# Optimization experiments

Measured on AMD Instinct MI355X. Metric: run time of the kernel, lower is better.

## Reference

```python
import jax, jax.numpy as jnp
import numpy as np

EPS = 1e-5  # BatchNorm1d default eps
DIMS = [(784, 1024), (1024, 1024), (1024, 1024), (1024, 10)]


def setup_inputs() -> dict:
    key = jax.random.key(0)
    ks = jax.random.split(key, 25)
    d = {"x": jax.random.normal(ks[0], (32768, 784), jnp.float32)}
    for i, (fi, fo) in enumerate(DIMS):
        j = i + 1
        base = 1 + 6 * i
        d[f"W{j}"] = jax.random.uniform(ks[base], (fo, fi), jnp.float32, -1.0, 1.0)
        d[f"b{j}"] = jnp.full((fo,), 0.01, jnp.float32)
        d[f"gamma{j}"] = jax.random.uniform(ks[base + 1], (fo,), jnp.float32, 0.5, 1.5)
        d[f"beta{j}"] = 0.1 * jax.random.normal(ks[base + 2], (fo,), jnp.float32)
        d[f"mean{j}"] = 0.1 * jax.random.normal(ks[base + 3], (fo,), jnp.float32)
        d[f"var{j}"] = jax.random.uniform(ks[base + 4], (fo,), jnp.float32, 0.5, 1.5)
    return d


def _bn(h, gamma, beta, mean, var):
    # inference-mode BatchNorm1d with running stats
    return gamma * (h - mean) * jax.lax.rsqrt(var + EPS) + beta


def reference(x,
              W1, b1, gamma1, beta1, mean1, var1,
              W2, b2, gamma2, beta2, mean2, var2,
              W3, b3, gamma3, beta3, mean3, var3,
              W4, b4, gamma4, beta4, mean4, var4):
    h = x.reshape(-1, 784)
    # layer 1: Quantizer(1) -> BinarizeLinear -> BN -> Hardtanh
    h = jnp.sign(h)
    h = h @ jnp.sign(W1).T + b1
    h = jnp.clip(_bn(h, gamma1, beta1, mean1, var1), -1.0, 1.0)
    # layer 2
    h = jnp.sign(h)
    h = h @ jnp.sign(W2).T + b2
    h = jnp.clip(_bn(h, gamma2, beta2, mean2, var2), -1.0, 1.0)
    # layer 3
    h = jnp.sign(h)
    h = h @ jnp.sign(W3).T + b3
    h = jnp.clip(_bn(h, gamma3, beta3, mean3, var3), -1.0, 1.0)
    # layer 4: Quantizer -> BinarizeLinear -> BN (no hardtanh)
    h = jnp.sign(h)
    h = h @ jnp.sign(W4).T + b4
    return _bn(h, gamma4, beta4, mean4, var4)
```

## Files before the change

### kernel.cpp

```cpp
#include <hip/hip_runtime.h>
#include <cstdint>
#include <climits>


typedef __attribute__((ext_vector_type(4))) int i32x4_t;

__device__ __forceinline__ void gload_lds16(const void* g, void* l) {
  __builtin_amdgcn_global_load_lds(
      (const __attribute__((address_space(1))) unsigned int*)g,
      (__attribute__((address_space(3))) unsigned int*)l, 16, 0, 0);
}

__device__ __forceinline__ int pack4(const float4 v) {
  int b0 = v.x > 0.f ? 1 : (v.x < 0.f ? -1 : 0);
  int b1 = v.y > 0.f ? 1 : (v.y < 0.f ? -1 : 0);
  int b2 = v.z > 0.f ? 1 : (v.z < 0.f ? -1 : 0);
  int b3 = v.w > 0.f ? 1 : (v.w < 0.f ? -1 : 0);
  return (b0 & 0xff) | ((b1 & 0xff) << 8) | ((b2 & 0xff) << 16) | (b3 << 24);
}


__global__ __launch_bounds__(256) void prep_mega_kernel(
    const float* __restrict__ x, int8_t* __restrict__ A0,
    const float* __restrict__ W1f, const float* __restrict__ W2f,
    const float* __restrict__ W3f, const float* __restrict__ W4f,
    int8_t* __restrict__ Wp1, int8_t* __restrict__ Wp2,
    int8_t* __restrict__ Wp3, int8_t* __restrict__ Wp4,
    const float* b1, const float* g1, const float* be1, const float* m1, const float* v1,
    const float* b2, const float* g2, const float* be2, const float* m2, const float* v2,
    const float* b3, const float* g3, const float* be3, const float* m3, const float* v3,
    const float* b4, const float* g4, const float* be4, const float* m4, const float* v4,
    int* __restrict__ T1, int* __restrict__ T2, int* __restrict__ T3,
    int8_t* __restrict__ S1, int8_t* __restrict__ S2, int8_t* __restrict__ S3,
    float* __restrict__ sc4, float* __restrict__ of4) {
  const int b = blockIdx.x;
  const int t = threadIdx.x;
  if (b < 32768) {
    const int col = t * 4;
    if (col < 784) {
      int packed = pack4(*(const float4*)(x + (size_t)b * 784 + col));
      *(int*)(A0 + (size_t)b * 832 + col) = packed;
    } else if (col < 832) {
      *(int*)(A0 + (size_t)b * 832 + col) = 0;
    }
  } else if (b < 35968) {
    const int b2i = b - 32768;
    const float* Wf; int8_t* Wp; int N, K, n, ost;
    if (b2i < 1024)      { Wf = W1f; Wp = Wp1; N = 1024; K = 784;  n = b2i;        ost = 832;  }
    else if (b2i < 2048) { Wf = W2f; Wp = Wp2; N = 1024; K = 1024; n = b2i - 1024; ost = 1024; }
    else if (b2i < 3072) { Wf = W3f; Wp = Wp3; N = 1024; K = 1024; n = b2i - 2048; ost = 1024; }
    else                 { Wf = W4f; Wp = Wp4; N = 10;   K = 1024; n = b2i - 3072; ost = 1024; }
    const int col = t * 4;
    if (col < ost) {
      int packed = 0;
      if (n < N && col + 3 < K)
        packed = pack4(*(const float4*)(Wf + (size_t)n * K + col));
      *(int*)(Wp + (size_t)n * ost + col) = packed;
    }
  } else {
    const int pb = b - 35968;
    if (pb < 12) {
      const int layer = pb >> 2;
      const int n = (pb & 3) * 256 + t;
      const float *bb, *gg, *be, *me, *va; int* T; int8_t* S;
      if (layer == 0)      { bb = b1; gg = g1; be = be1; me = m1; va = v1; T = T1; S = S1; }
      else if (layer == 1) { bb = b2; gg = g2; be = be2; me = m2; va = v2; T = T2; S = S2; }
      else                 { bb = b3; gg = g3; be = be3; me = m3; va = v3; T = T3; S = S3; }
      double g = (double)gg[n];
      double rs = 1.0 / sqrt((double)va[n] + 1e-5);
      int th; int8_t s;
      if (g > 0.0) {
        double tv = (double)me[n] - (double)bb[n] - (double)be[n] / (g * rs);
        tv = fmin(fmax(tv, -2.0e9), 2.0e9);
        th = (int)floor(tv) + 1; s = 1;
      } else if (g < 0.0) {
        double tv = (double)me[n] - (double)bb[n] - (double)be[n] / (g * rs);
        tv = fmin(fmax(tv, -2.0e9), 2.0e9);
        th = (int)ceil(tv); s = -1;
      } else {
        th = INT_MIN; s = (be[n] > 0.f) ? (int8_t)1 : (int8_t)-1;
      }
      T[n] = th; S[n] = s;
    } else if (t < 10) {
      double rs = 1.0 / sqrt((double)v4[t] + 1e-5);
      double sd = (double)g4[t] * rs;
      sc4[t] = (float)sd;
      of4[t] = (float)(sd * ((double)b4[t] - (double)m4[t]) + (double)be4[t]);
    }
  }
}

template <int FINAL>
__global__ __launch_bounds__(256) void gemm_bnn_kernel(
    const int8_t* __restrict__ A, const int8_t* __restrict__ W,
    int ldk, int nkt,
    const int* __restrict__ T, const int8_t* __restrict__ S,
    const float* __restrict__ scale, const float* __restrict__ offs,
    int8_t* __restrict__ Aout, float* __restrict__ out) {
  __shared__ i32x4_t smem[2048];
  int8_t* sm = (int8_t*)smem;
  const int tid = threadIdx.x;
  const int lane = tid & 63;
  const int w = tid >> 6;
  const int wrow = w >> 1, wcol = w & 1;
  const int row0 = blockIdx.x * 128;
  const int col0 = blockIdx.y * 128;

  const int jj0 = tid, jj1 = tid + 256;
  const int r0 = jj0 >> 2, r1 = jj1 >> 2;
  const int s0 = (jj0 & 3) ^ ((r0 >> 1) & 3);
  const int s1 = (jj1 & 3) ^ ((r1 >> 1) & 3);
  const int8_t* aS0 = A + (size_t)(row0 + r0) * ldk + s0 * 16;
  const int8_t* aS1 = A + (size_t)(row0 + r1) * ldk + s1 * 16;
  const int8_t* bS0 = W + (size_t)(col0 + r0) * ldk + s0 * 16;
  const int8_t* bS1 = W + (size_t)(col0 + r1) * ldk + s1 * 16;
  const int dA0 = jj0 * 16, dA1 = jj1 * 16;
  const int dB0 = 8192 + jj0 * 16, dB1 = 8192 + jj1 * 16;

  int a_off[4], b_off[4];
#pragma unroll
  for (int i = 0; i < 4; ++i) {
    int ra = wrow * 64 + i * 16 + (lane & 15);
    a_off[i] = ra * 64 + ((((lane >> 4) ^ (ra >> 1)) & 3) << 4);
    int rb = wcol * 64 + i * 16 + (lane & 15);
    b_off[i] = 8192 + rb * 64 + ((((lane >> 4) ^ (rb >> 1)) & 3) << 4);
  }

  i32x4_t acc[4][4];
#pragma unroll
  for (int m = 0; m < 4; ++m)
#pragma unroll
    for (int n = 0; n < 4; ++n) acc[m][n] = (i32x4_t){0, 0, 0, 0};

  gload_lds16(aS0, sm + dA0);
  gload_lds16(aS1, sm + dA1);
  gload_lds16(bS0, sm + dB0);
  gload_lds16(bS1, sm + dB1);

  for (int kt = 0; kt < nkt - 1; ++kt) {
    aS0 += 64; aS1 += 64; bS0 += 64; bS1 += 64;
    int8_t* smw = sm + (((kt + 1) & 1) << 14);
    gload_lds16(aS0, smw + dA0);
    gload_lds16(aS1, smw + dA1);
    gload_lds16(bS0, smw + dB0);
    gload_lds16(bS1, smw + dB1);
    asm volatile("s_waitcnt vmcnt(4)" ::: "memory");
    __builtin_amdgcn_s_barrier();
    const int8_t* smr = sm + ((kt & 1) << 14);
    i32x4_t av[4], bv[4];
#pragma unroll
    for (int i = 0; i < 4; ++i) av[i] = *(const i32x4_t*)(smr + a_off[i]);
#pragma unroll
    for (int i = 0; i < 4; ++i) bv[i] = *(const i32x4_t*)(smr + b_off[i]);
#pragma unroll
    for (int m = 0; m < 4; ++m)
#pragma unroll
      for (int n = 0; n < 4; ++n)
        acc[m][n] = __builtin_amdgcn_mfma_i32_16x16x64_i8(av[m], bv[n], acc[m][n], 0, 0, 0);
    __builtin_amdgcn_s_barrier();
  }
  asm volatile("s_waitcnt vmcnt(0)" ::: "memory");
  __builtin_amdgcn_s_barrier();
  {
    const int8_t* smr = sm + (((nkt - 1) & 1) << 14);
    i32x4_t av[4], bv[4];
#pragma unroll
    for (int i = 0; i < 4; ++i) av[i] = *(const i32x4_t*)(smr + a_off[i]);
#pragma unroll
    for (int i = 0; i < 4; ++i) bv[i] = *(const i32x4_t*)(smr + b_off[i]);
#pragma unroll
    for (int m = 0; m < 4; ++m)
#pragma unroll
      for (int n = 0; n < 4; ++n)
        acc[m][n] = __builtin_amdgcn_mfma_i32_16x16x64_i8(av[m], bv[n], acc[m][n], 0, 0, 0);
  }

  if (FINAL == 0) {
#pragma unroll
    for (int n = 0; n < 4; ++n) {
      const int oc = col0 + wcol * 64 + n * 16 + (lane & 15);
      const int tn = T[oc];
      const int8_t sn = S[oc];
#pragma unroll
      for (int m = 0; m < 4; ++m) {
        const int orb = row0 + wrow * 64 + m * 16 + ((lane >> 4) << 2);
#pragma unroll
        for (int r = 0; r < 4; ++r) {
          int8_t v = (acc[m][n][r] >= tn) ? sn : (int8_t)(-sn);
          Aout[(size_t)(orb + r) * 1024 + oc] = v;
        }
      }
    }
  } else {
#pragma unroll
    for (int n = 0; n < 4; ++n) {
      const int oc = col0 + wcol * 64 + n * 16 + (lane & 15);
      if (oc < 10) {
        const float sc = scale[oc], of = offs[oc];
#pragma unroll
        for (int m = 0; m < 4; ++m) {
          const int orb = row0 + wrow * 64 + m * 16 + ((lane >> 4) << 2);
#pragma unroll
          for (int r = 0; r < 4; ++r)
            out[(size_t)(orb + r) * 10 + oc] = sc * (float)acc[m][n][r] + of;
        }
      }
    }
  }
}


#define A0_STRIDE 28

__global__ __launch_bounds__(256) void pack_w_kernel(
    const float* __restrict__ W, uint32_t* __restrict__ Wp,
    int nout, int K, int wstride) {
  int idx = blockIdx.x * blockDim.x + threadIdx.x;
  if (idx >= nout * wstride) return;
  int n = idx / wstride;
  int wi = idx - n * wstride;
  const float* wr = W + (size_t)n * K;
  uint32_t word = 0;
  int base = wi * 32;
  for (int i = 0; i < 32; ++i) {
    int c = base + i;
    if (c < K && wr[c] > 0.f) word |= (1u << i);
  }
  Wp[idx] = word;
}

__global__ __launch_bounds__(256) void prep_thr_kernel(
    const float* __restrict__ b, const float* __restrict__ gamma,
    const float* __restrict__ beta, const float* __restrict__ mean,
    const float* __restrict__ var, int K, int N,
    int* __restrict__ thr, uint32_t* __restrict__ flipm) {
  int n = blockIdx.x * blockDim.x + threadIdx.x;
  if (n >= N) return;
  double g = (double)gamma[n];
  double rs = 1.0 / sqrt((double)var[n] + 1e-5);
  int th;
  if (g != 0.0) {
    double t = (double)mean[n] - (double)b[n] - (double)beta[n] / (g * rs);
    double pt = ((double)K - t) * 0.5;
    th = (g > 0.0) ? (int)ceil(pt) : ((int)floor(pt) + 1);
  } else {
    th = (beta[n] > 0.f) ? (K + 2) : -1;
  }
  thr[n] = th;
  if ((n & 31) == 0) {
    uint32_t m = 0;
    for (int i = 0; i < 32 && (n + i) < N; ++i)
      if (gamma[n + i] < 0.f) m |= (1u << i);
    flipm[n >> 5] = m;
  }
}

__global__ __launch_bounds__(64) void prep_out_kernel(
    const float* __restrict__ b, const float* __restrict__ gamma,
    const float* __restrict__ beta, const float* __restrict__ mean,
    const float* __restrict__ var, int N,
    float* __restrict__ s, float* __restrict__ o) {
  int n = threadIdx.x;
  if (n >= N) return;
  double rs = 1.0 / sqrt((double)var[n] + 1e-5);
  double sd = (double)gamma[n] * rs;
  s[n] = (float)sd;
  o[n] = (float)(sd * ((double)b[n] - (double)mean[n]) + (double)beta[n]);
}

__global__ __launch_bounds__(256) void pack_a_kernel(
    const float* __restrict__ x, uint32_t* __restrict__ A0) {
  int gt = blockIdx.x * blockDim.x + threadIdx.x;
  int wv = gt >> 6;
  int lane = gt & 63;
  int row = wv / 13;
  int seg = wv - row * 13;
  int col = (seg << 6) + lane;
  bool pred = (col < 784) && (x[(size_t)row * 784 + col] > 0.f);
  unsigned long long m = __ballot(pred);
  int widx = seg * 2;
  if (lane == 0)
    A0[(size_t)row * A0_STRIDE + widx] = (uint32_t)m;
  else if (lane == 1 && widx + 1 < 25)
    A0[(size_t)row * A0_STRIDE + widx + 1] = (uint32_t)(m >> 32);
}

__device__ __forceinline__ void layer1024(
    uint32_t a[32], const uint32_t* __restrict__ Wp,
    const int* __restrict__ thr, const uint32_t* __restrict__ fm,
    uint32_t* lds, int lane, int w) {
  const int nb = w * 128;
  uint32_t word = 0;
#pragma unroll 2
  for (int ni = 0; ni < 128; ++ni) {
    const int n = nb + ni;
    const uint32_t* __restrict__ wp = Wp + n * 32;
    uint32_t p0 = 0, p1 = 0, p2 = 0, p3 = 0;
#pragma unroll
    for (int k = 0; k < 32; k += 4) {
      p0 += __popc(a[k + 0] ^ wp[k + 0]);
      p1 += __popc(a[k + 1] ^ wp[k + 1]);
      p2 += __popc(a[k + 2] ^ wp[k + 2]);
      p3 += __popc(a[k + 3] ^ wp[k + 3]);
    }
    int p = (int)(p0 + p1 + p2 + p3);
    word |= ((p < thr[n]) ? 1u : 0u) << (ni & 31);
    if ((ni & 31) == 31) {
      lds[lane * 33 + (n >> 5)] = word ^ fm[n >> 5];
      word = 0;
    }
  }
  __syncthreads();
#pragma unroll
  for (int k = 0; k < 32; ++k) a[k] = lds[lane * 33 + k];
  __syncthreads();
}

__global__ __launch_bounds__(512, 4) void fused_kernel(
    const uint32_t* __restrict__ A0,
    const uint32_t* __restrict__ Wp1, const int* __restrict__ thr1, const uint32_t* __restrict__ fm1,
    const uint32_t* __restrict__ Wp2, const int* __restrict__ thr2, const uint32_t* __restrict__ fm2,
    const uint32_t* __restrict__ Wp3, const int* __restrict__ thr3, const uint32_t* __restrict__ fm3,
    const uint32_t* __restrict__ Wp4, const float* __restrict__ s4, const float* __restrict__ o4,
    float* __restrict__ out) {
  __shared__ uint32_t lds[64 * 33];
  const int lane = threadIdx.x & 63;
  const int w = __builtin_amdgcn_readfirstlane((int)(threadIdx.x >> 6));
  const int row = blockIdx.x * 64 + lane;

  uint32_t a[32];
  {
    const uint4* A4 = (const uint4*)(A0 + (size_t)row * A0_STRIDE);
#pragma unroll
    for (int i = 0; i < 7; ++i) {
      uint4 q = A4[i];
      a[4 * i + 0] = q.x; a[4 * i + 1] = q.y; a[4 * i + 2] = q.z; a[4 * i + 3] = q.w;
    }
  }
  {
    const int nb = w * 128;
    uint32_t word = 0;
#pragma unroll 2
    for (int ni = 0; ni < 128; ++ni) {
      const int n = nb + ni;
      const uint32_t* __restrict__ wp = Wp1 + n * A0_STRIDE;
      uint32_t p0 = 0, p1 = 0, p2 = 0, p3 = 0;
#pragma unroll
      for (int k = 0; k < 24; k += 4) {
        p0 += __popc(a[k + 0] ^ wp[k + 0]);
        p1 += __popc(a[k + 1] ^ wp[k + 1]);
        p2 += __popc(a[k + 2] ^ wp[k + 2]);
        p3 += __popc(a[k + 3] ^ wp[k + 3]);
      }
      p0 += __popc(a[24] ^ wp[24]);
      int p = (int)(p0 + p1 + p2 + p3);
      word |= ((p < thr1[n]) ? 1u : 0u) << (ni & 31);
      if ((ni & 31) == 31) {
        lds[lane * 33 + (n >> 5)] = word ^ fm1[n >> 5];
        word = 0;
      }
    }
    __syncthreads();
#pragma unroll
    for (int k = 0; k < 32; ++k) a[k] = lds[lane * 33 + k];
    __syncthreads();
  }
  layer1024(a, Wp2, thr2, fm2, lds, lane, w);
  layer1024(a, Wp3, thr3, fm3, lds, lane, w);
  for (int j = w; j < 10; j += 8) {
    const uint32_t* __restrict__ wp = Wp4 + j * 32;
    uint32_t p0 = 0, p1 = 0, p2 = 0, p3 = 0;
#pragma unroll
    for (int k = 0; k < 32; k += 4) {
      p0 += __popc(a[k + 0] ^ wp[k + 0]);
      p1 += __popc(a[k + 1] ^ wp[k + 1]);
      p2 += __popc(a[k + 2] ^ wp[k + 2]);
      p3 += __popc(a[k + 3] ^ wp[k + 3]);
    }
    float dotf = 1024.f - 2.f * (float)(p0 + p1 + p2 + p3);
    out[(size_t)row * 10 + j] = s4[j] * dotf + o4[j];
  }
}

extern "C" void kernel_launch(void* const* d_in, const int* in_sizes, int n_in,
                              void* d_out, int out_size, void* d_ws, size_t ws_size,
                              hipStream_t stream) {
  const float* x   = (const float*)d_in[0];
  const float* W1  = (const float*)d_in[1];
  const float* b1  = (const float*)d_in[2];
  const float* g1  = (const float*)d_in[3];
  const float* be1 = (const float*)d_in[4];
  const float* m1  = (const float*)d_in[5];
  const float* v1  = (const float*)d_in[6];
  const float* W2  = (const float*)d_in[7];
  const float* b2  = (const float*)d_in[8];
  const float* g2  = (const float*)d_in[9];
  const float* be2 = (const float*)d_in[10];
  const float* m2  = (const float*)d_in[11];
  const float* v2  = (const float*)d_in[12];
  const float* W3  = (const float*)d_in[13];
  const float* b3  = (const float*)d_in[14];
  const float* g3  = (const float*)d_in[15];
  const float* be3 = (const float*)d_in[16];
  const float* m3  = (const float*)d_in[17];
  const float* v3  = (const float*)d_in[18];
  const float* W4  = (const float*)d_in[19];
  const float* b4  = (const float*)d_in[20];
  const float* g4  = (const float*)d_in[21];
  const float* be4 = (const float*)d_in[22];
  const float* m4  = (const float*)d_in[23];
  const float* v4  = (const float*)d_in[24];
  float* outp = (float*)d_out;
  (void)in_sizes; (void)n_in; (void)out_size;

  uint8_t* ws = (uint8_t*)d_ws;
  const size_t NEED = 100ULL << 20;

  if (ws_size >= NEED) {
    size_t off = 0;
    int8_t* A0  = (int8_t*)(ws + off); off += (size_t)32768 * 832;
    int8_t* Bp1 = (int8_t*)(ws + off); off += (size_t)32768 * 1024;
    int8_t* Bp2 = (int8_t*)(ws + off); off += (size_t)32768 * 1024;
    int8_t* Wp1 = (int8_t*)(ws + off); off += (size_t)1024 * 832;
    int8_t* Wp2 = (int8_t*)(ws + off); off += (size_t)1024 * 1024;
    int8_t* Wp3 = (int8_t*)(ws + off); off += (size_t)1024 * 1024;
    int8_t* Wp4 = (int8_t*)(ws + off); off += (size_t)128 * 1024;
    int* T1     = (int*)(ws + off);    off += 4096;
    int* T2     = (int*)(ws + off);    off += 4096;
    int* T3     = (int*)(ws + off);    off += 4096;
    int8_t* S1  = (int8_t*)(ws + off); off += 1024;
    int8_t* S2  = (int8_t*)(ws + off); off += 1024;
    int8_t* S3  = (int8_t*)(ws + off); off += 1024;
    float* sc4  = (float*)(ws + off);  off += 512;
    float* of4  = (float*)(ws + off);  off += 512;

    prep_mega_kernel<<<35981, 256, 0, stream>>>(
        x, A0, W1, W2, W3, W4, Wp1, Wp2, Wp3, Wp4,
        b1, g1, be1, m1, v1, b2, g2, be2, m2, v2,
        b3, g3, be3, m3, v3, b4, g4, be4, m4, v4,
        T1, T2, T3, S1, S2, S3, sc4, of4);

    gemm_bnn_kernel<0><<<dim3(256, 8), 256, 0, stream>>>(
        A0, Wp1, 832, 13, T1, S1, nullptr, nullptr, Bp1, nullptr);
    gemm_bnn_kernel<0><<<dim3(256, 8), 256, 0, stream>>>(
        Bp1, Wp2, 1024, 16, T2, S2, nullptr, nullptr, Bp2, nullptr);
    gemm_bnn_kernel<0><<<dim3(256, 8), 256, 0, stream>>>(
        Bp2, Wp3, 1024, 16, T3, S3, nullptr, nullptr, Bp1, nullptr);
    gemm_bnn_kernel<1><<<dim3(256, 1), 256, 0, stream>>>(
        Bp1, Wp4, 1024, 16, nullptr, nullptr, sc4, of4, nullptr, outp);
  } else {
    size_t off = 0;
    uint32_t* A0  = (uint32_t*)(ws + off); off += (size_t)32768 * A0_STRIDE * 4;
    uint32_t* Wp1 = (uint32_t*)(ws + off); off += (size_t)1024 * A0_STRIDE * 4;
    uint32_t* Wp2 = (uint32_t*)(ws + off); off += (size_t)1024 * 32 * 4;
    uint32_t* Wp3 = (uint32_t*)(ws + off); off += (size_t)1024 * 32 * 4;
    uint32_t* Wp4 = (uint32_t*)(ws + off); off += 4096;
    int* thr1     = (int*)(ws + off);      off += 4096;
    int* thr2     = (int*)(ws + off);      off += 4096;
    int* thr3     = (int*)(ws + off);      off += 4096;
    uint32_t* fm1 = (uint32_t*)(ws + off); off += 128;
    uint32_t* fm2 = (uint32_t*)(ws + off); off += 128;
    uint32_t* fm3 = (uint32_t*)(ws + off); off += 128;
    float* s4o    = (float*)(ws + off);    off += 64;
    float* o4o    = (float*)(ws + off);    off += 64;

    pack_w_kernel<<<(1024 * A0_STRIDE + 255) / 256, 256, 0, stream>>>(W1, Wp1, 1024, 784, A0_STRIDE);
    pack_w_kernel<<<(1024 * 32 + 255) / 256, 256, 0, stream>>>(W2, Wp2, 1024, 1024, 32);
    pack_w_kernel<<<(1024 * 32 + 255) / 256, 256, 0, stream>>>(W3, Wp3, 1024, 1024, 32);
    pack_w_kernel<<<(10 * 32 + 255) / 256, 256, 0, stream>>>(W4, Wp4, 10, 1024, 32);
    prep_thr_kernel<<<4, 256, 0, stream>>>(b1, g1, be1, m1, v1, 784, 1024, thr1, fm1);
    prep_thr_kernel<<<4, 256, 0, stream>>>(b2, g2, be2, m2, v2, 1024, 1024, thr2, fm2);
    prep_thr_kernel<<<4, 256, 0, stream>>>(b3, g3, be3, m3, v3, 1024, 1024, thr3, fm3);
    prep_out_kernel<<<1, 64, 0, stream>>>(b4, g4, be4, m4, v4, 10, s4o, o4o);
    pack_a_kernel<<<(32768 * 13) / 4, 256, 0, stream>>>(x, A0);
    fused_kernel<<<512, 512, 0, stream>>>(A0, Wp1, thr1, fm1, Wp2, thr2, fm2,
                                          Wp3, thr3, fm3, Wp4, s4o, o4o, outp);
  }
}
```

Before: 345.8 us.

## Use 256x256 tiles with 512-thread blocks and grid swizzle for hidden BNN GEMMs

Replaces the 128x128-tile int8 MFMA GEMM for the three hidden layers with a 256x256-tile kernel of 8 waves, each computing a 128x64 sub-tile, using double-buffered 64 KB LDS. A block-index swizzle groups blocks that share A rows and W columns to improve L2 reuse. The larger tiles halve global/LDS traffic per MFMA but raise register pressure (32 accumulators per wave) and cut the grid to 512 blocks, which may lower occupancy. The final layer is split into its own non-templated kernel.

```diff
diff --git a/kernel.cpp b/kernel.cpp
--- a/kernel.cpp
+++ b/kernel.cpp
@@ -90,13 +90,117 @@
   }
 }
 
-template <int FINAL>
-__global__ __launch_bounds__(256) void gemm_bnn_kernel(
+__global__ __launch_bounds__(512) void gemm_bnn256_kernel(
     const int8_t* __restrict__ A, const int8_t* __restrict__ W,
     int ldk, int nkt,
     const int* __restrict__ T, const int8_t* __restrict__ S,
+    int8_t* __restrict__ Aout) {
+  __shared__ i32x4_t smem[4096];
+  int8_t* sm = (int8_t*)smem;
+  const int tid = threadIdx.x;
+  const int lane = tid & 63;
+  const int w = tid >> 6;
+  const int wm = w >> 2, wn = w & 3;
+
+  const int bid = blockIdx.x;
+  const int swz = (bid & 7) * 64 + (bid >> 3);
+  const int row0 = (swz >> 2) * 256;
+  const int col0 = (swz & 3) * 256;
+
+  const int jj0 = tid, jj1 = tid + 512;
+  const int r0 = jj0 >> 2, r1 = jj1 >> 2;
+  const int s0 = (jj0 & 3) ^ ((r0 >> 1) & 3);
+  const int s1 = (jj1 & 3) ^ ((r1 >> 1) & 3);
+  const int8_t* aS0 = A + (size_t)(row0 + r0) * ldk + s0 * 16;
+  const int8_t* aS1 = A + (size_t)(row0 + r1) * ldk + s1 * 16;
+  const int8_t* bS0 = W + (size_t)(col0 + r0) * ldk + s0 * 16;
+  const int8_t* bS1 = W + (size_t)(col0 + r1) * ldk + s1 * 16;
+  const int dA0 = jj0 * 16, dA1 = jj1 * 16;
+  const int dB0 = 16384 + jj0 * 16, dB1 = 16384 + jj1 * 16;
+
+  int a_off[8], b_off[4];
+#pragma unroll
+  for (int m = 0; m < 8; ++m) {
+    int ra = wm * 128 + m * 16 + (lane & 15);
+    a_off[m] = ra * 64 + ((((lane >> 4) ^ (ra >> 1)) & 3) << 4);
+  }
+#pragma unroll
+  for (int n = 0; n < 4; ++n) {
+    int rb = wn * 64 + n * 16 + (lane & 15);
+    b_off[n] = 16384 + rb * 64 + ((((lane >> 4) ^ (rb >> 1)) & 3) << 4);
+  }
+
+  i32x4_t acc[8][4];
+#pragma unroll
+  for (int m = 0; m < 8; ++m)
+#pragma unroll
+    for (int n = 0; n < 4; ++n) acc[m][n] = (i32x4_t){0, 0, 0, 0};
+
+  gload_lds16(aS0, sm + dA0);
+  gload_lds16(aS1, sm + dA1);
+  gload_lds16(bS0, sm + dB0);
+  gload_lds16(bS1, sm + dB1);
+
+  for (int kt = 0; kt < nkt - 1; ++kt) {
+    aS0 += 64; aS1 += 64; bS0 += 64; bS1 += 64;
+    int8_t* smw = sm + (((kt + 1) & 1) << 15);
+    gload_lds16(aS0, smw + dA0);
+    gload_lds16(aS1, smw + dA1);
+    gload_lds16(bS0, smw + dB0);
+    gload_lds16(bS1, smw + dB1);
+    asm volatile("s_waitcnt vmcnt(4)" ::: "memory");
+    __builtin_amdgcn_s_barrier();
+    const int8_t* smr = sm + ((kt & 1) << 15);
+    i32x4_t av[8], bv[4];
+#pragma unroll
+    for (int i = 0; i < 8; ++i) av[i] = *(const i32x4_t*)(smr + a_off[i]);
+#pragma unroll
+    for (int i = 0; i < 4; ++i) bv[i] = *(const i32x4_t*)(smr + b_off[i]);
+#pragma unroll
+    for (int m = 0; m < 8; ++m)
+#pragma unroll
+      for (int n = 0; n < 4; ++n)
+        acc[m][n] = __builtin_amdgcn_mfma_i32_16x16x64_i8(av[m], bv[n], acc[m][n], 0, 0, 0);
+    __builtin_amdgcn_s_barrier();
+  }
+  asm volatile("s_waitcnt vmcnt(0)" ::: "memory");
+  __builtin_amdgcn_s_barrier();
+  {
+    const int8_t* smr = sm + (((nkt - 1) & 1) << 15);
+    i32x4_t av[8], bv[4];
+#pragma unroll
+    for (int i = 0; i < 8; ++i) av[i] = *(const i32x4_t*)(smr + a_off[i]);
+#pragma unroll
+    for (int i = 0; i < 4; ++i) bv[i] = *(const i32x4_t*)(smr + b_off[i]);
+#pragma unroll
+    for (int m = 0; m < 8; ++m)
+#pragma unroll
+      for (int n = 0; n < 4; ++n)
+        acc[m][n] = __builtin_amdgcn_mfma_i32_16x16x64_i8(av[m], bv[n], acc[m][n], 0, 0, 0);
+  }
+
+#pragma unroll
+  for (int n = 0; n < 4; ++n) {
+    const int oc = col0 + wn * 64 + n * 16 + (lane & 15);
+    const int tn = T[oc];
+    const int8_t sn = S[oc];
+#pragma unroll
+    for (int m = 0; m < 8; ++m) {
+      const int orb = row0 + wm * 128 + m * 16 + ((lane >> 4) << 2);
+#pragma unroll
+      for (int r = 0; r < 4; ++r) {
+        int8_t v = (acc[m][n][r] >= tn) ? sn : (int8_t)(-sn);
+        Aout[(size_t)(orb + r) * 1024 + oc] = v;
+      }
+    }
+  }
+}
+
+__global__ __launch_bounds__(256) void gemm_final_kernel(
+    const int8_t* __restrict__ A, const int8_t* __restrict__ W,
+    int ldk, int nkt,
     const float* __restrict__ scale, const float* __restrict__ offs,
-    int8_t* __restrict__ Aout, float* __restrict__ out) {
+    float* __restrict__ out) {
   __shared__ i32x4_t smem[2048];
   int8_t* sm = (int8_t*)smem;
   const int tid = threadIdx.x;
@@ -104,7 +208,7 @@
   const int w = tid >> 6;
   const int wrow = w >> 1, wcol = w & 1;
   const int row0 = blockIdx.x * 128;
-  const int col0 = blockIdx.y * 128;
+  const int col0 = 0;
 
   const int jj0 = tid, jj1 = tid + 256;
   const int r0 = jj0 >> 2, r1 = jj1 >> 2;
@@ -175,35 +279,17 @@
         acc[m][n] = __builtin_amdgcn_mfma_i32_16x16x64_i8(av[m], bv[n], acc[m][n], 0, 0, 0);
   }
 
-  if (FINAL == 0) {
-#pragma unroll
-    for (int n = 0; n < 4; ++n) {
-      const int oc = col0 + wcol * 64 + n * 16 + (lane & 15);
-      const int tn = T[oc];
-      const int8_t sn = S[oc];
+#pragma unroll
+  for (int n = 0; n < 4; ++n) {
+    const int oc = col0 + wcol * 64 + n * 16 + (lane & 15);
+    if (oc < 10) {
+      const float sc = scale[oc], of = offs[oc];
 #pragma unroll
       for (int m = 0; m < 4; ++m) {
         const int orb = row0 + wrow * 64 + m * 16 + ((lane >> 4) << 2);
 #pragma unroll
-        for (int r = 0; r < 4; ++r) {
-          int8_t v = (acc[m][n][r] >= tn) ? sn : (int8_t)(-sn);
-          Aout[(size_t)(orb + r) * 1024 + oc] = v;
-        }
-      }
-    }
-  } else {
-#pragma unroll
-    for (int n = 0; n < 4; ++n) {
-      const int oc = col0 + wcol * 64 + n * 16 + (lane & 15);
-      if (oc < 10) {
-        const float sc = scale[oc], of = offs[oc];
-#pragma unroll
-        for (int m = 0; m < 4; ++m) {
-          const int orb = row0 + wrow * 64 + m * 16 + ((lane >> 4) << 2);
-#pragma unroll
-          for (int r = 0; r < 4; ++r)
-            out[(size_t)(orb + r) * 10 + oc] = sc * (float)acc[m][n][r] + of;
-        }
+        for (int r = 0; r < 4; ++r)
+          out[(size_t)(orb + r) * 10 + oc] = sc * (float)acc[m][n][r] + of;
       }
     }
   }
@@ -440,14 +526,10 @@
         b3, g3, be3, m3, v3, b4, g4, be4, m4, v4,
         T1, T2, T3, S1, S2, S3, sc4, of4);
 
-    gemm_bnn_kernel<0><<<dim3(256, 8), 256, 0, stream>>>(
-        A0, Wp1, 832, 13, T1, S1, nullptr, nullptr, Bp1, nullptr);
-    gemm_bnn_kernel<0><<<dim3(256, 8), 256, 0, stream>>>(
-        Bp1, Wp2, 1024, 16, T2, S2, nullptr, nullptr, Bp2, nullptr);
-    gemm_bnn_kernel<0><<<dim3(256, 8), 256, 0, stream>>>(
-        Bp2, Wp3, 1024, 16, T3, S3, nullptr, nullptr, Bp1, nullptr);
-    gemm_bnn_kernel<1><<<dim3(256, 1), 256, 0, stream>>>(
-        Bp1, Wp4, 1024, 16, nullptr, nullptr, sc4, of4, nullptr, outp);
+    gemm_bnn256_kernel<<<512, 512, 0, stream>>>(A0, Wp1, 832, 13, T1, S1, Bp1);
+    gemm_bnn256_kernel<<<512, 512, 0, stream>>>(Bp1, Wp2, 1024, 16, T2, S2, Bp2);
+    gemm_bnn256_kernel<<<512, 512, 0, stream>>>(Bp2, Wp3, 1024, 16, T3, S3, Bp1);
+    gemm_final_kernel<<<256, 256, 0, stream>>>(Bp1, Wp4, 1024, 16, sc4, of4, outp);
   } else {
     size_t off = 0;
     uint32_t* A0  = (uint32_t*)(ws + off); off += (size_t)32768 * A0_STRIDE * 4;
```

Result: faster. 324.0 us (-6.3%).

## Fuse all four binary MLP layers into one kernel keeping activations in LDS

Applied to the files above, without the earlier changes.

Replaces the four separate int8 MFMA GEMM launches with a single fused kernel. Each block owns 32 rows and keeps the binarized activations in a 64KB double buffer in LDS across all layers. Weights are pre-packed into an MFMA fragment-ready layout so each wave can load B fragments directly from global memory with register double-buffering. This removes the global round-trips of the intermediate 32MB activation tensors and three kernel launches. The cost is that every block re-streams the full weight set from L2, blocks are small (32 rows), and the large LDS footprint limits occupancy.

```diff
diff --git a/kernel.cpp b/kernel.cpp
--- a/kernel.cpp
+++ b/kernel.cpp
@@ -24,8 +24,8 @@
     const float* __restrict__ x, int8_t* __restrict__ A0,
     const float* __restrict__ W1f, const float* __restrict__ W2f,
     const float* __restrict__ W3f, const float* __restrict__ W4f,
-    int8_t* __restrict__ Wp1, int8_t* __restrict__ Wp2,
-    int8_t* __restrict__ Wp3, int8_t* __restrict__ Wp4,
+    int8_t* __restrict__ Wf1, int8_t* __restrict__ Wf2,
+    int8_t* __restrict__ Wf3, int8_t* __restrict__ Wf4,
     const float* b1, const float* g1, const float* be1, const float* m1, const float* v1,
     const float* b2, const float* g2, const float* be2, const float* m2, const float* v2,
     const float* b3, const float* g3, const float* be3, const float* m3, const float* v3,
@@ -43,22 +43,36 @@
     } else if (col < 832) {
       *(int*)(A0 + (size_t)b * 832 + col) = 0;
     }
-  } else if (b < 35968) {
+  } else if (b < 35648) {
     const int b2i = b - 32768;
-    const float* Wf; int8_t* Wp; int N, K, n, ost;
-    if (b2i < 1024)      { Wf = W1f; Wp = Wp1; N = 1024; K = 784;  n = b2i;        ost = 832;  }
-    else if (b2i < 2048) { Wf = W2f; Wp = Wp2; N = 1024; K = 1024; n = b2i - 1024; ost = 1024; }
-    else if (b2i < 3072) { Wf = W3f; Wp = Wp3; N = 1024; K = 1024; n = b2i - 2048; ost = 1024; }
-    else                 { Wf = W4f; Wp = Wp4; N = 10;   K = 1024; n = b2i - 3072; ost = 1024; }
-    const int col = t * 4;
-    if (col < ost) {
-      int packed = 0;
-      if (n < N && col + 3 < K)
-        packed = pack4(*(const float4*)(Wf + (size_t)n * K + col));
-      *(int*)(Wp + (size_t)n * ost + col) = packed;
-    }
+    const float* Wf; int8_t* Wo; int Kreal, blk;
+    if (b2i < 832)        { Wf = W1f; Wo = Wf1; Kreal = 784;  blk = b2i;        }
+    else if (b2i < 1856)  { Wf = W2f; Wo = Wf2; Kreal = 1024; blk = b2i - 832;  }
+    else                  { Wf = W3f; Wo = Wf3; Kreal = 1024; blk = b2i - 1856; }
+    const int o = (blk * 256 + t) * 4;
+    const int j  = o & 15;
+    const int l6 = (o >> 4) & 63;
+    const int cb = (o >> 10) & 63;
+    const int kt = o >> 16;
+    const int colw = cb * 16 + (l6 & 15);
+    const int k = kt * 64 + ((l6 >> 4) << 4) + j;
+    int packed = 0;
+    if (k < Kreal)
+      packed = pack4(*(const float4*)(Wf + (size_t)colw * Kreal + k));
+    *(int*)(Wo + o) = packed;
+  } else if (b < 35664) {
+    const int o = ((b - 35648) * 256 + t) * 4;
+    const int j  = o & 15;
+    const int l6 = (o >> 4) & 63;
+    const int kt = o >> 10;
+    const int colw = l6 & 15;
+    const int k = kt * 64 + ((l6 >> 4) << 4) + j;
+    int packed = 0;
+    if (colw < 10)
+      packed = pack4(*(const float4*)(W4f + (size_t)colw * 1024 + k));
+    *(int*)(Wf4 + o) = packed;
   } else {
-    const int pb = b - 35968;
+    const int pb = b - 35664;
     if (pb < 12) {
       const int layer = pb >> 2;
       const int n = (pb & 3) * 256 + t;
@@ -90,120 +104,127 @@
   }
 }
 
-template <int FINAL>
-__global__ __launch_bounds__(256) void gemm_bnn_kernel(
-    const int8_t* __restrict__ A, const int8_t* __restrict__ W,
-    int ldk, int nkt,
+__device__ __forceinline__ void do_layer(
+    const int8_t* lin, int8_t* lout, int nkt,
+    const int8_t* __restrict__ Wf,
     const int* __restrict__ T, const int8_t* __restrict__ S,
-    const float* __restrict__ scale, const float* __restrict__ offs,
-    int8_t* __restrict__ Aout, float* __restrict__ out) {
-  __shared__ i32x4_t smem[2048];
-  int8_t* sm = (int8_t*)smem;
+    int lane, int wn) {
+  for (int p = 0; p < 4; ++p) {
+    int a_off[2];
+#pragma unroll
+    for (int m = 0; m < 2; ++m) {
+      const int row = m * 16 + (lane & 15);
+      a_off[m] = row * 1024 + ((((lane >> 4) ^ (row >> 1)) & 3) << 4);
+    }
+    const int8_t* bq = Wf + ((size_t)(p * 16 + wn * 4)) * 1024 + lane * 16;
+    i32x4_t acc[2][4];
+#pragma unroll
+    for (int m = 0; m < 2; ++m)
+#pragma unroll
+      for (int n = 0; n < 4; ++n) acc[m][n] = (i32x4_t){0, 0, 0, 0};
+    i32x4_t bvA[4], bvB[4];
+#pragma unroll
+    for (int n = 0; n < 4; ++n) bvA[n] = *(const i32x4_t*)(bq + n * 1024);
+
+#define FSTEP(KT, BVC, BVN)                                                   \
+    {                                                                         \
+      const int kt_ = (KT);                                                   \
+      if (kt_ + 1 < nkt) {                                                    \
+        _Pragma("unroll")                                                     \
+        for (int n = 0; n < 4; ++n)                                           \
+          BVN[n] = *(const i32x4_t*)(bq + (size_t)(kt_ + 1) * 65536 + n * 1024); \
+        asm volatile("s_waitcnt vmcnt(4)" ::: "memory");                      \
+      } else {                                                                \
+        asm volatile("s_waitcnt vmcnt(0)" ::: "memory");                      \
+      }                                                                       \
+      i32x4_t av[2];                                                          \
+      _Pragma("unroll")                                                       \
+      for (int m = 0; m < 2; ++m)                                             \
+        av[m] = *(const i32x4_t*)(lin + a_off[m] + kt_ * 64);                 \
+      _Pragma("unroll")                                                       \
+      for (int m = 0; m < 2; ++m)                                             \
+        _Pragma("unroll")                                                     \
+        for (int n = 0; n < 4; ++n)                                           \
+          acc[m][n] = __builtin_amdgcn_mfma_i32_16x16x64_i8(av[m], BVC[n], acc[m][n], 0, 0, 0); \
+    }
+
+    int kt = 0;
+    for (; kt + 2 <= nkt; kt += 2) { FSTEP(kt, bvA, bvB); FSTEP(kt + 1, bvB, bvA); }
+    if (kt < nkt) FSTEP(kt, bvA, bvB);
+#undef FSTEP
+
+#pragma unroll
+    for (int n = 0; n < 4; ++n) {
+      const int oc = p * 256 + wn * 64 + n * 16 + (lane & 15);
+      const int tn = T[oc];
+      const int8_t snn = S[oc];
+#pragma unroll
+      for (int m = 0; m < 2; ++m)
+#pragma unroll
+        for (int r = 0; r < 4; ++r) {
+          const int row = m * 16 + ((lane >> 4) << 2) + r;
+          const int slot = (n ^ (row >> 1)) & 3;
+          lout[row * 1024 + p * 256 + wn * 64 + (slot << 4) + (lane & 15)] =
+              (acc[m][n][r] >= tn) ? snn : (int8_t)(-snn);
+        }
+    }
+  }
+}
+
+__global__ __launch_bounds__(256, 2) void fused_mlp_kernel(
+    const int8_t* __restrict__ A0,
+    const int8_t* __restrict__ Wf1, const int8_t* __restrict__ Wf2,
+    const int8_t* __restrict__ Wf3, const int8_t* __restrict__ Wf4,
+    const int* __restrict__ T1, const int8_t* __restrict__ S1,
+    const int* __restrict__ T2, const int8_t* __restrict__ S2,
+    const int* __restrict__ T3, const int8_t* __restrict__ S3,
+    const float* __restrict__ sc4, const float* __restrict__ of4,
+    float* __restrict__ out) {
+  __shared__ int8_t smf[65536];
+  int8_t* buf0 = smf;
+  int8_t* buf1 = smf + 32768;
   const int tid = threadIdx.x;
   const int lane = tid & 63;
-  const int w = tid >> 6;
-  const int wrow = w >> 1, wcol = w & 1;
-  const int row0 = blockIdx.x * 128;
-  const int col0 = blockIdx.y * 128;
-
-  const int jj0 = tid, jj1 = tid + 256;
-  const int r0 = jj0 >> 2, r1 = jj1 >> 2;
-  const int s0 = (jj0 & 3) ^ ((r0 >> 1) & 3);
-  const int s1 = (jj1 & 3) ^ ((r1 >> 1) & 3);
-  const int8_t* aS0 = A + (size_t)(row0 + r0) * ldk + s0 * 16;
-  const int8_t* aS1 = A + (size_t)(row0 + r1) * ldk + s1 * 16;
-  const int8_t* bS0 = W + (size_t)(col0 + r0) * ldk + s0 * 16;
-  const int8_t* bS1 = W + (size_t)(col0 + r1) * ldk + s1 * 16;
-  const int dA0 = jj0 * 16, dA1 = jj1 * 16;
-  const int dB0 = 8192 + jj0 * 16, dB1 = 8192 + jj1 * 16;
-
-  int a_off[4], b_off[4];
-#pragma unroll
-  for (int i = 0; i < 4; ++i) {
-    int ra = wrow * 64 + i * 16 + (lane & 15);
-    a_off[i] = ra * 64 + ((((lane >> 4) ^ (ra >> 1)) & 3) << 4);
-    int rb = wcol * 64 + i * 16 + (lane & 15);
-    b_off[i] = 8192 + rb * 64 + ((((lane >> 4) ^ (rb >> 1)) & 3) << 4);
-  }
-
-  i32x4_t acc[4][4];
-#pragma unroll
-  for (int m = 0; m < 4; ++m)
-#pragma unroll
-    for (int n = 0; n < 4; ++n) acc[m][n] = (i32x4_t){0, 0, 0, 0};
-
-  gload_lds16(aS0, sm + dA0);
-  gload_lds16(aS1, sm + dA1);
-  gload_lds16(bS0, sm + dB0);
-  gload_lds16(bS1, sm + dB1);
-
-  for (int kt = 0; kt < nkt - 1; ++kt) {
-    aS0 += 64; aS1 += 64; bS0 += 64; bS1 += 64;
-    int8_t* smw = sm + (((kt + 1) & 1) << 14);
-    gload_lds16(aS0, smw + dA0);
-    gload_lds16(aS1, smw + dA1);
-    gload_lds16(bS0, smw + dB0);
-    gload_lds16(bS1, smw + dB1);
-    asm volatile("s_waitcnt vmcnt(4)" ::: "memory");
-    __builtin_amdgcn_s_barrier();
-    const int8_t* smr = sm + ((kt & 1) << 14);
-    i32x4_t av[4], bv[4];
-#pragma unroll
-    for (int i = 0; i < 4; ++i) av[i] = *(const i32x4_t*)(smr + a_off[i]);
-#pragma unroll
-    for (int i = 0; i < 4; ++i) bv[i] = *(const i32x4_t*)(smr + b_off[i]);
-#pragma unroll
-    for (int m = 0; m < 4; ++m)
-#pragma unroll
-      for (int n = 0; n < 4; ++n)
-        acc[m][n] = __builtin_amdgcn_mfma_i32_16x16x64_i8(av[m], bv[n], acc[m][n], 0, 0, 0);
-    __builtin_amdgcn_s_barrier();
-  }
-  asm volatile("s_waitcnt vmcnt(0)" ::: "memory");
-  __builtin_amdgcn_s_barrier();
-  {
-    const int8_t* smr = sm + (((nkt - 1) & 1) << 14);
-    i32x4_t av[4], bv[4];
-#pragma unroll
-    for (int i = 0; i < 4; ++i) av[i] = *(const i32x4_t*)(smr + a_off[i]);
-#pragma unroll
-    for (int i = 0; i < 4; ++i) bv[i] = *(const i32x4_t*)(smr + b_off[i]);
-#pragma unroll
-    for (int m = 0; m < 4; ++m)
-#pragma unroll
-      for (int n = 0; n < 4; ++n)
-        acc[m][n] = __builtin_amdgcn_mfma_i32_16x16x64_i8(av[m], bv[n], acc[m][n], 0, 0, 0);
-  }
-
-  if (FINAL == 0) {
-#pragma unroll
-    for (int n = 0; n < 4; ++n) {
-      const int oc = col0 + wcol * 64 + n * 16 + (lane & 15);
-      const int tn = T[oc];
-      const int8_t sn = S[oc];
-#pragma unroll
-      for (int m = 0; m < 4; ++m) {
-        const int orb = row0 + wrow * 64 + m * 16 + ((lane >> 4) << 2);
-#pragma unroll
-        for (int r = 0; r < 4; ++r) {
-          int8_t v = (acc[m][n][r] >= tn) ? sn : (int8_t)(-sn);
-          Aout[(size_t)(orb + r) * 1024 + oc] = v;
-        }
-      }
-    }
-  } else {
-#pragma unroll
-    for (int n = 0; n < 4; ++n) {
-      const int oc = col0 + wcol * 64 + n * 16 + (lane & 15);
-      if (oc < 10) {
-        const float sc = scale[oc], of = offs[oc];
-#pragma unroll
-        for (int m = 0; m < 4; ++m) {
-          const int orb = row0 + wrow * 64 + m * 16 + ((lane >> 4) << 2);
-#pragma unroll
-          for (int r = 0; r < 4; ++r)
-            out[(size_t)(orb + r) * 10 + oc] = sc * (float)acc[m][n][r] + of;
-        }
+  const int wn = tid >> 6;
+  const int row0 = blockIdx.x * 32;
+
+#pragma unroll
+  for (int i = 0; i < 8; ++i) {
+    const int g = tid + 256 * i;
+    const int row = g >> 6;
+    const int sw = (row >> 1) & 3;
+    const int sp = g & 3;
+    const int k64 = (g >> 2) & 15;
+    const int8_t* src = A0 + (size_t)(row0 + row) * 832 + k64 * 64 + (((sp ^ sw) & 3) << 4);
+    gload_lds16(src, smf + g * 16);
+  }
+  __syncthreads();
+
+  do_layer(buf0, buf1, 13, Wf1, T1, S1, lane, wn);
+  __syncthreads();
+  do_layer(buf1, buf0, 16, Wf2, T2, S2, lane, wn);
+  __syncthreads();
+  do_layer(buf0, buf1, 16, Wf3, T3, S3, lane, wn);
+  __syncthreads();
+
+  if (wn < 2) {
+    const int row = wn * 16 + (lane & 15);
+    const int a4 = row * 1024 + ((((lane >> 4) ^ (row >> 1)) & 3) << 4);
+    i32x4_t acc4 = (i32x4_t){0, 0, 0, 0};
+    const int8_t* bq = Wf4 + lane * 16;
+#pragma unroll
+    for (int kt = 0; kt < 16; ++kt) {
+      i32x4_t bv = *(const i32x4_t*)(bq + kt * 1024);
+      i32x4_t av = *(const i32x4_t*)(buf1 + a4 + kt * 64);
+      acc4 = __builtin_amdgcn_mfma_i32_16x16x64_i8(av, bv, acc4, 0, 0, 0);
+    }
+    const int col = lane & 15;
+    if (col < 10) {
+      const float sc = sc4[col], of = of4[col];
+#pragma unroll
+      for (int r = 0; r < 4; ++r) {
+        const int orow = wn * 16 + ((lane >> 4) << 2) + r;
+        out[(size_t)(row0 + orow) * 10 + col] = sc * (float)acc4[r] + of;
       }
     }
   }
@@ -414,17 +435,15 @@
   (void)in_sizes; (void)n_in; (void)out_size;
 
   uint8_t* ws = (uint8_t*)d_ws;
-  const size_t NEED = 100ULL << 20;
+  const size_t NEED = 64ULL << 20;
 
   if (ws_size >= NEED) {
     size_t off = 0;
     int8_t* A0  = (int8_t*)(ws + off); off += (size_t)32768 * 832;
-    int8_t* Bp1 = (int8_t*)(ws + off); off += (size_t)32768 * 1024;
-    int8_t* Bp2 = (int8_t*)(ws + off); off += (size_t)32768 * 1024;
-    int8_t* Wp1 = (int8_t*)(ws + off); off += (size_t)1024 * 832;
-    int8_t* Wp2 = (int8_t*)(ws + off); off += (size_t)1024 * 1024;
-    int8_t* Wp3 = (int8_t*)(ws + off); off += (size_t)1024 * 1024;
-    int8_t* Wp4 = (int8_t*)(ws + off); off += (size_t)128 * 1024;
+    int8_t* Wf1 = (int8_t*)(ws + off); off += (size_t)13 * 64 * 1024;
+    int8_t* Wf2 = (int8_t*)(ws + off); off += (size_t)16 * 64 * 1024;
+    int8_t* Wf3 = (int8_t*)(ws + off); off += (size_t)16 * 64 * 1024;
+    int8_t* Wf4 = (int8_t*)(ws + off); off += 16384;
     int* T1     = (int*)(ws + off);    off += 4096;
     int* T2     = (int*)(ws + off);    off += 4096;
     int* T3     = (int*)(ws + off);    off += 4096;
@@ -434,20 +453,14 @@
     float* sc4  = (float*)(ws + off);  off += 512;
     float* of4  = (float*)(ws + off);  off += 512;
 
-    prep_mega_kernel<<<35981, 256, 0, stream>>>(
-        x, A0, W1, W2, W3, W4, Wp1, Wp2, Wp3, Wp4,
+    prep_mega_kernel<<<35677, 256, 0, stream>>>(
+        x, A0, W1, W2, W3, W4, Wf1, Wf2, Wf3, Wf4,
         b1, g1, be1, m1, v1, b2, g2, be2, m2, v2,
         b3, g3, be3, m3, v3, b4, g4, be4, m4, v4,
         T1, T2, T3, S1, S2, S3, sc4, of4);
 
-    gemm_bnn_kernel<0><<<dim3(256, 8), 256, 0, stream>>>(
-        A0, Wp1, 832, 13, T1, S1, nullptr, nullptr, Bp1, nullptr);
-    gemm_bnn_kernel<0><<<dim3(256, 8), 256, 0, stream>>>(
-        Bp1, Wp2, 1024, 16, T2, S2, nullptr, nullptr, Bp2, nullptr);
-    gemm_bnn_kernel<0><<<dim3(256, 8), 256, 0, stream>>>(
-        Bp2, Wp3, 1024, 16, T3, S3, nullptr, nullptr, Bp1, nullptr);
-    gemm_bnn_kernel<1><<<dim3(256, 1), 256, 0, stream>>>(
-        Bp1, Wp4, 1024, 16, nullptr, nullptr, sc4, of4, nullptr, outp);
+    fused_mlp_kernel<<<1024, 256, 0, stream>>>(
+        A0, Wf1, Wf2, Wf3, Wf4, T1, S1, T2, S2, T3, S3, sc4, of4, outp);
   } else {
     size_t off = 0;
     uint32_t* A0  = (uint32_t*)(ws + off); off += (size_t)32768 * A0_STRIDE * 4;
```

New measurement: 316.1 us. 8.6% less time.
